# Kernel tuning notes

Hardware: AMD Instinct MI355X
Metric: run time of the kernel (lower is better)

The kernel has to match this reference:

```python
import jax, jax.numpy as jnp
import numpy as np

TEMP = 0.5
EPS = 1e-8  # torch CosineSimilarity eps


def setup_inputs() -> dict:
    key = jax.random.key(0)
    k1, k2 = jax.random.split(key)
    B, D = 4096, 256
    return {
        "features1": jax.random.normal(k1, (B, D), dtype=jnp.float32),
        "features2": jax.random.normal(k2, (B, D), dtype=jnp.float32),
    }


def reference(features1, features2):
    B = features1.shape[0]
    f = jnp.concatenate([features1, features2], axis=0)  # [2B, D]
    # cosine similarity matrix via norms + GEMM (same math as broadcasted cos)
    n = jnp.sqrt(jnp.sum(f * f, axis=-1))  # [2B]
    dots = f @ f.T  # [2B, 2B]
    logits = dots / jnp.maximum(n[:, None] * n[None, :], EPS) / TEMP
    # labels = cat([arange(B), arange(B)]) -- faithful to the source module
    labels = jnp.concatenate([jnp.arange(B), jnp.arange(B)], axis=0)  # [2B]
    lse = jax.nn.logsumexp(logits, axis=1)  # [2B]
    picked = logits[jnp.arange(2 * B), labels]  # [2B]
    return jnp.mean(lse - picked)
```

## Files before the change

### kernel.cpp

```cpp
#include <hip/hip_runtime.h>
#include <hip/hip_bf16.h>
#include <math.h>


#define B_ROWS 4096
#define D_DIM  256
#define N_ROWS 8192
#define NPANEL 64
#define NTRI   2080

typedef __attribute__((ext_vector_type(8))) short short8;
typedef __attribute__((ext_vector_type(4))) float f32x4;

__device__ __forceinline__ float bf2f(unsigned short u) {
  union { unsigned int i; float f; } p; p.i = ((unsigned int)u) << 16; return p.f;
}

__global__ __launch_bounds__(256) void nt_normalize(const float* __restrict__ f1,
                                                    const float* __restrict__ f2,
                                                    unsigned short* __restrict__ G) {
  const int row  = blockIdx.x * 4 + (threadIdx.x >> 6);
  const int lane = threadIdx.x & 63;
  const float* src = (row < B_ROWS) ? (f1 + (size_t)row * D_DIM)
                                    : (f2 + (size_t)(row - B_ROWS) * D_DIM);
  float4 v = reinterpret_cast<const float4*>(src)[lane];
  float ss = v.x * v.x + v.y * v.y + v.z * v.z + v.w * v.w;
#pragma unroll
  for (int m = 1; m < 64; m <<= 1) ss += __shfl_xor(ss, m, 64);
  float scale = 1.41421356237309515f * rsqrtf(fmaxf(ss, 1e-30f));
  union { ushort4 u; __hip_bfloat16 h[4]; } p;
  p.h[0] = __float2bfloat16(v.x * scale);
  p.h[1] = __float2bfloat16(v.y * scale);
  p.h[2] = __float2bfloat16(v.z * scale);
  p.h[3] = __float2bfloat16(v.w * scale);
  reinterpret_cast<ushort4*>(G + (size_t)row * D_DIM)[lane] = p.u;
}

__global__ __launch_bounds__(256) void nt_picked(const unsigned short* __restrict__ G,
                                                 float* __restrict__ picked) {
  const int row  = blockIdx.x * 4 + (threadIdx.x >> 6);
  const int lane = threadIdx.x & 63;
  const int lbl  = (row < B_ROWS) ? row : (row - B_ROWS);
  ushort4 a = reinterpret_cast<const ushort4*>(G + (size_t)row * D_DIM)[lane];
  ushort4 b = reinterpret_cast<const ushort4*>(G + (size_t)lbl * D_DIM)[lane];
  float s = bf2f(a.x) * bf2f(b.x) + bf2f(a.y) * bf2f(b.y) +
            bf2f(a.z) * bf2f(b.z) + bf2f(a.w) * bf2f(b.w);
#pragma unroll
  for (int m = 1; m < 64; m <<= 1) s += __shfl_xor(s, m, 64);
  if (lane == 0) picked[row] = s;
}

__device__ __forceinline__ void stage_lds(const char* gsrc_base, char* lds_base,
                                          int rounds, int tid) {
  const int lane = tid & 63, wid = tid >> 6;
  for (int r = 0; r < rounds; ++r) {
    const int o  = r * 4096 + wid * 1024 + lane * 16;
    const int so = o ^ (((o >> 9) & 7) << 4);
    __builtin_amdgcn_global_load_lds(
        (const __attribute__((address_space(1))) void*)(gsrc_base + so),
        (__attribute__((address_space(3))) void*)(lds_base + r * 4096 + wid * 1024),
        16, 0, 0);
  }
}

__global__ __launch_bounds__(256, 2) void nt_gemm_tri(
    const unsigned short* __restrict__ G,
    float* __restrict__ partial)
{
  int bid = (blockIdx.x & 7) * (NTRI / 8) + (blockIdx.x >> 3);
  int rb = (int)((sqrtf(8.f * (float)bid + 1.f) - 1.f) * 0.5f);
  while ((rb + 1) * (rb + 2) / 2 <= bid) ++rb;
  while (rb * (rb + 1) / 2 > bid) --rb;
  const int cb = bid - rb * (rb + 1) / 2;

  const int tid  = threadIdx.x;
  const int lane = tid & 63;
  const int wid  = tid >> 6;
  const int wr   = wid >> 1;
  const int wc   = wid & 1;

  __shared__ short8 lds8[4096];
  char* ldsb = reinterpret_cast<char*>(lds8);
  const char* gb = reinterpret_cast<const char*>(G);

  stage_lds(gb + (size_t)rb * 128 * 512, ldsb, 16, tid);
  __syncthreads();

  short8 afrag[4][8];
  {
    const int r0 = wr * 64;
#pragma unroll
    for (int m = 0; m < 4; ++m) {
      const int row = r0 + m * 16 + (lane & 15);
      const int sw  = (row & 7) << 4;
#pragma unroll
      for (int ks = 0; ks < 8; ++ks) {
        const int off = (row * 512 + ks * 64 + ((lane >> 4) << 4)) ^ sw;
        afrag[m][ks] = *reinterpret_cast<const short8*>(ldsb + off);
      }
    }
  }
  __syncthreads();

  stage_lds(gb + (size_t)cb * 128 * 512, ldsb, 16, tid);
  f32x4 acc[4][4] = {};
  __syncthreads();

#pragma unroll
  for (int ks = 0; ks < 8; ++ks) {
    short8 bfrag[4];
#pragma unroll
    for (int n = 0; n < 4; ++n) {
      const int brow = wc * 64 + n * 16 + (lane & 15);
      const int off  = (brow * 512 + ks * 64 + ((lane >> 4) << 4)) ^ ((brow & 7) << 4);
      bfrag[n] = *reinterpret_cast<const short8*>(ldsb + off);
    }
#pragma unroll
    for (int m = 0; m < 4; ++m)
#pragma unroll
      for (int n = 0; n < 4; ++n)
        acc[m][n] = __builtin_amdgcn_mfma_f32_16x16x32_bf16(
            afrag[m][ks], bfrag[n], acc[m][n], 0, 0, 0);
  }

  float rs[16], cs[4];
#pragma unroll
  for (int i = 0; i < 16; ++i) rs[i] = 0.f;
#pragma unroll
  for (int n = 0; n < 4; ++n) cs[n] = 0.f;
#pragma unroll
  for (int m = 0; m < 4; ++m)
#pragma unroll
    for (int n = 0; n < 4; ++n)
#pragma unroll
      for (int j = 0; j < 4; ++j) {
        const float e = __expf(acc[m][n][j]);
        rs[m * 4 + j] += e;
        cs[n] += e;
      }
#pragma unroll
  for (int i = 0; i < 16; ++i) {
    float s = rs[i];
    s += __shfl_xor(s, 1, 64);
    s += __shfl_xor(s, 2, 64);
    s += __shfl_xor(s, 4, 64);
    s += __shfl_xor(s, 8, 64);
    rs[i] = s;
  }
#pragma unroll
  for (int n = 0; n < 4; ++n) {
    float s = cs[n];
    s += __shfl_xor(s, 16, 64);
    s += __shfl_xor(s, 32, 64);
    cs[n] = s;
  }
  __syncthreads();
  float* redr = reinterpret_cast<float*>(ldsb);
  float* redc = reinterpret_cast<float*>(ldsb + 1024);
  if ((lane & 15) == 0) {
    const int g = lane >> 4;
#pragma unroll
    for (int i = 0; i < 16; ++i)
      redr[wc * 128 + wr * 64 + (i >> 2) * 16 + g * 4 + (i & 3)] = rs[i];
  }
  if ((lane >> 4) == 0) {
#pragma unroll
    for (int n = 0; n < 4; ++n)
      redc[wr * 128 + wc * 64 + n * 16 + lane] = cs[n];
  }
  __syncthreads();
  if (tid < 128) {
    const float v = redr[tid] + redr[128 + tid];
    partial[(size_t)cb * N_ROWS + (size_t)rb * 128 + tid] = v;
  } else if (rb != cb) {
    const int t = tid - 128;
    const float v = redc[t] + redc[128 + t];
    partial[(size_t)rb * N_ROWS + (size_t)cb * 128 + t] = v;
  }
}

__global__ __launch_bounds__(128) void nt_finalize1(const float* __restrict__ partial,
                                                    const float* __restrict__ picked,
                                                    float* __restrict__ loss_part) {
  const int b = blockIdx.x, tid = threadIdx.x;
  const int r = b * 128 + tid;
  float s = 0.f;
#pragma unroll
  for (int c = 0; c < NPANEL; ++c) s += partial[(size_t)c * N_ROWS + r];
  float local = __logf(s) - picked[r];
#pragma unroll
  for (int m = 1; m < 64; m <<= 1) local += __shfl_xor(local, m, 64);
  __shared__ float red[2];
  if ((tid & 63) == 0) red[tid >> 6] = local;
  __syncthreads();
  if (tid == 0) loss_part[b] = red[0] + red[1];
}

__global__ __launch_bounds__(64) void nt_finalize2(const float* __restrict__ loss_part,
                                                   float* __restrict__ out) {
  const int tid = threadIdx.x;
  float v = loss_part[tid];
#pragma unroll
  for (int m = 1; m < 64; m <<= 1) v += __shfl_xor(v, m, 64);
  if (tid == 0) out[0] = v / (float)N_ROWS;
}

extern "C" void kernel_launch(void* const* d_in, const int* in_sizes, int n_in,
                              void* d_out, int out_size, void* d_ws, size_t ws_size,
                              hipStream_t stream) {
  const float* f1 = (const float*)d_in[0];
  const float* f2 = (const float*)d_in[1];
  float* out = (float*)d_out;

  char* ws = (char*)d_ws;
  unsigned short* G = (unsigned short*)ws;
  float* partial   = (float*)(ws + (size_t)4 * 1024 * 1024);
  float* picked    = (float*)(ws + (size_t)6 * 1024 * 1024);
  float* loss_part = (float*)(ws + (size_t)6 * 1024 * 1024 + 32 * 1024);

  hipLaunchKernelGGL(nt_normalize, dim3(N_ROWS / 4), dim3(256), 0, stream, f1, f2, G);
  hipLaunchKernelGGL(nt_picked,    dim3(N_ROWS / 4), dim3(256), 0, stream, G, picked);
  hipLaunchKernelGGL(nt_gemm_tri,  dim3(NTRI),       dim3(256), 0, stream, G, partial);
  hipLaunchKernelGGL(nt_finalize1, dim3(NPANEL),     dim3(128), 0, stream, partial, picked, loss_part);
  hipLaunchKernelGGL(nt_finalize2, dim3(1),          dim3(64),  0, stream, loss_part, out);
}
```

Measured before the change: 65.90 us.

## Fuse normalize with picked logits and reuse A panel across column chunks

The normalize and picked kernels are merged into one, which computes the cross-pair dot product from fp32 values held in shared memory. The diagonal picked term for the first half becomes the constant 2. The triangular GEMM now gives each block one row panel and a chunk of up to eight column panels. The A fragments stay in registers while B sub-tiles of 64 rows are double-buffered in LDS, which cuts the repeated A staging and the number of blocks. Column sums go into a larger partial buffer that the finalize kernel reduces. The grid shrinks to 512 blocks with uneven work per block, which risks load imbalance and a lower share of active CUs.

```diff
diff --git a/kernel.cpp b/kernel.cpp
--- a/kernel.cpp
+++ b/kernel.cpp
@@ -7,47 +7,41 @@
 #define D_DIM  256
 #define N_ROWS 8192
 #define NPANEL 64
-#define NTRI   2080
 
 typedef __attribute__((ext_vector_type(8))) short short8;
 typedef __attribute__((ext_vector_type(4))) float f32x4;
 
-__device__ __forceinline__ float bf2f(unsigned short u) {
-  union { unsigned int i; float f; } p; p.i = ((unsigned int)u) << 16; return p.f;
-}
-
-__global__ __launch_bounds__(256) void nt_normalize(const float* __restrict__ f1,
-                                                    const float* __restrict__ f2,
-                                                    unsigned short* __restrict__ G) {
-  const int row  = blockIdx.x * 4 + (threadIdx.x >> 6);
-  const int lane = threadIdx.x & 63;
-  const float* src = (row < B_ROWS) ? (f1 + (size_t)row * D_DIM)
-                                    : (f2 + (size_t)(row - B_ROWS) * D_DIM);
-  float4 v = reinterpret_cast<const float4*>(src)[lane];
+__global__ __launch_bounds__(256) void nt_norm_picked(
+    const float* __restrict__ f1, const float* __restrict__ f2,
+    unsigned short* __restrict__ G, float* __restrict__ picked_cross) {
+  __shared__ float4 vbuf[2][64];
+  __shared__ float ssbuf[2];
+  const int tid = threadIdx.x, lane = tid & 63, w = tid >> 6;
+  const int pl = w >> 1, src = w & 1;
+  const int p = blockIdx.x * 2 + pl;
+  const float* rowp = (src == 0 ? f1 : f2) + (size_t)p * D_DIM;
+  float4 v = reinterpret_cast<const float4*>(rowp)[lane];
   float ss = v.x * v.x + v.y * v.y + v.z * v.z + v.w * v.w;
 #pragma unroll
   for (int m = 1; m < 64; m <<= 1) ss += __shfl_xor(ss, m, 64);
-  float scale = 1.41421356237309515f * rsqrtf(fmaxf(ss, 1e-30f));
-  union { ushort4 u; __hip_bfloat16 h[4]; } p;
-  p.h[0] = __float2bfloat16(v.x * scale);
-  p.h[1] = __float2bfloat16(v.y * scale);
-  p.h[2] = __float2bfloat16(v.z * scale);
-  p.h[3] = __float2bfloat16(v.w * scale);
-  reinterpret_cast<ushort4*>(G + (size_t)row * D_DIM)[lane] = p.u;
-}
-
-__global__ __launch_bounds__(256) void nt_picked(const unsigned short* __restrict__ G,
-                                                 float* __restrict__ picked) {
-  const int row  = blockIdx.x * 4 + (threadIdx.x >> 6);
-  const int lane = threadIdx.x & 63;
-  const int lbl  = (row < B_ROWS) ? row : (row - B_ROWS);
-  ushort4 a = reinterpret_cast<const ushort4*>(G + (size_t)row * D_DIM)[lane];
-  ushort4 b = reinterpret_cast<const ushort4*>(G + (size_t)lbl * D_DIM)[lane];
-  float s = bf2f(a.x) * bf2f(b.x) + bf2f(a.y) * bf2f(b.y) +
-            bf2f(a.z) * bf2f(b.z) + bf2f(a.w) * bf2f(b.w);
-#pragma unroll
-  for (int m = 1; m < 64; m <<= 1) s += __shfl_xor(s, m, 64);
-  if (lane == 0) picked[row] = s;
+  const float scale = 1.41421356237309515f * rsqrtf(fmaxf(ss, 1e-30f));
+  union { ushort4 u; __hip_bfloat16 h[4]; } pk;
+  pk.h[0] = __float2bfloat16(v.x * scale);
+  pk.h[1] = __float2bfloat16(v.y * scale);
+  pk.h[2] = __float2bfloat16(v.z * scale);
+  pk.h[3] = __float2bfloat16(v.w * scale);
+  const int grow = p + src * B_ROWS;
+  reinterpret_cast<ushort4*>(G + (size_t)grow * D_DIM)[lane] = pk.u;
+  if (src == 0) { vbuf[pl][lane] = v; if (lane == 0) ssbuf[pl] = ss; }
+  __syncthreads();
+  if (src == 1) {
+    float4 u = vbuf[pl][lane];
+    float d = v.x * u.x + v.y * u.y + v.z * u.z + v.w * u.w;
+#pragma unroll
+    for (int m = 1; m < 64; m <<= 1) d += __shfl_xor(d, m, 64);
+    if (lane == 0)
+      picked_cross[p] = 2.0f * d * rsqrtf(ss) * rsqrtf(ssbuf[pl]);
+  }
 }
 
 __device__ __forceinline__ void stage_lds(const char* gsrc_base, char* lds_base,
@@ -67,11 +61,12 @@
     const unsigned short* __restrict__ G,
     float* __restrict__ partial)
 {
-  int bid = (blockIdx.x & 7) * (NTRI / 8) + (blockIdx.x >> 3);
-  int rb = (int)((sqrtf(8.f * (float)bid + 1.f) - 1.f) * 0.5f);
-  while ((rb + 1) * (rb + 2) / 2 <= bid) ++rb;
-  while (rb * (rb + 1) / 2 > bid) --rb;
-  const int cb = bid - rb * (rb + 1) / 2;
+  const int bid = blockIdx.x;
+  const int rb  = 63 - (bid >> 3);
+  const int ch  = bid & 7;
+  const int cb0 = ch << 3;
+  if (cb0 > rb) return;
+  const int nsub = (rb + 1 - cb0 < 8 ? rb + 1 - cb0 : 8) << 1;
 
   const int tid  = threadIdx.x;
   const int lane = tid & 63;
@@ -83,9 +78,8 @@
   char* ldsb = reinterpret_cast<char*>(lds8);
   const char* gb = reinterpret_cast<const char*>(G);
 
-  stage_lds(gb + (size_t)rb * 128 * 512, ldsb, 16, tid);
-  __syncthreads();
-
+  stage_lds(gb + (size_t)rb * 65536, ldsb, 16, tid);
+  __syncthreads();
   short8 afrag[4][8];
   {
     const int r0 = wr * 64;
@@ -102,102 +96,107 @@
   }
   __syncthreads();
 
-  stage_lds(gb + (size_t)cb * 128 * 512, ldsb, 16, tid);
-  f32x4 acc[4][4] = {};
-  __syncthreads();
-
-#pragma unroll
-  for (int ks = 0; ks < 8; ++ks) {
-    short8 bfrag[4];
-#pragma unroll
-    for (int n = 0; n < 4; ++n) {
-      const int brow = wc * 64 + n * 16 + (lane & 15);
-      const int off  = (brow * 512 + ks * 64 + ((lane >> 4) << 4)) ^ ((brow & 7) << 4);
-      bfrag[n] = *reinterpret_cast<const short8*>(ldsb + off);
+  float rs[16];
+#pragma unroll
+  for (int i = 0; i < 16; ++i) rs[i] = 0.f;
+
+  stage_lds(gb + (size_t)cb0 * 65536, ldsb, 8, tid);
+  __syncthreads();
+
+  for (int s = 0; s < nsub; ++s) {
+    if (s + 1 < nsub)
+      stage_lds(gb + (size_t)cb0 * 65536 + (size_t)(s + 1) * 32768,
+                ldsb + ((s + 1) & 1) * 32768, 8, tid);
+
+    const char* bbuf = ldsb + (s & 1) * 32768;
+    f32x4 acc[4][2] = {};
+#pragma unroll
+    for (int ks = 0; ks < 8; ++ks) {
+      short8 bfrag[2];
+#pragma unroll
+      for (int n = 0; n < 2; ++n) {
+        const int brow = wc * 32 + n * 16 + (lane & 15);
+        const int off  = (brow * 512 + ks * 64 + ((lane >> 4) << 4)) ^ ((brow & 7) << 4);
+        bfrag[n] = *reinterpret_cast<const short8*>(bbuf + off);
+      }
+#pragma unroll
+      for (int m = 0; m < 4; ++m)
+#pragma unroll
+        for (int n = 0; n < 2; ++n)
+          acc[m][n] = __builtin_amdgcn_mfma_f32_16x16x32_bf16(
+              afrag[m][ks], bfrag[n], acc[m][n], 0, 0, 0);
     }
+    float cs0 = 0.f, cs1 = 0.f;
 #pragma unroll
     for (int m = 0; m < 4; ++m)
 #pragma unroll
-      for (int n = 0; n < 4; ++n)
-        acc[m][n] = __builtin_amdgcn_mfma_f32_16x16x32_bf16(
-            afrag[m][ks], bfrag[n], acc[m][n], 0, 0, 0);
-  }
-
-  float rs[16], cs[4];
-#pragma unroll
-  for (int i = 0; i < 16; ++i) rs[i] = 0.f;
-#pragma unroll
-  for (int n = 0; n < 4; ++n) cs[n] = 0.f;
-#pragma unroll
-  for (int m = 0; m < 4; ++m)
-#pragma unroll
-    for (int n = 0; n < 4; ++n)
-#pragma unroll
       for (int j = 0; j < 4; ++j) {
-        const float e = __expf(acc[m][n][j]);
-        rs[m * 4 + j] += e;
-        cs[n] += e;
-      }
+        const float e0 = __expf(acc[m][0][j]);
+        const float e1 = __expf(acc[m][1][j]);
+        rs[m * 4 + j] += e0 + e1;
+        cs0 += e0; cs1 += e1;
+      }
+    const int cb = cb0 + (s >> 1);
+    if (cb != rb) {
+      cs0 += __shfl_xor(cs0, 16, 64); cs0 += __shfl_xor(cs0, 32, 64);
+      cs1 += __shfl_xor(cs1, 16, 64); cs1 += __shfl_xor(cs1, 32, 64);
+      if (lane < 16) {
+        float* dst = partial + (size_t)(8 + 2 * rb + wr) * N_ROWS
+                   + cb0 * 128 + s * 64 + wc * 32 + lane;
+        dst[0]  = cs0;
+        dst[16] = cs1;
+      }
+    }
+    __syncthreads();
+  }
+
 #pragma unroll
   for (int i = 0; i < 16; ++i) {
-    float s = rs[i];
-    s += __shfl_xor(s, 1, 64);
-    s += __shfl_xor(s, 2, 64);
-    s += __shfl_xor(s, 4, 64);
-    s += __shfl_xor(s, 8, 64);
-    rs[i] = s;
-  }
-#pragma unroll
-  for (int n = 0; n < 4; ++n) {
-    float s = cs[n];
-    s += __shfl_xor(s, 16, 64);
-    s += __shfl_xor(s, 32, 64);
-    cs[n] = s;
+    float v = rs[i];
+    v += __shfl_xor(v, 1, 64);
+    v += __shfl_xor(v, 2, 64);
+    v += __shfl_xor(v, 4, 64);
+    v += __shfl_xor(v, 8, 64);
+    rs[i] = v;
   }
   __syncthreads();
   float* redr = reinterpret_cast<float*>(ldsb);
-  float* redc = reinterpret_cast<float*>(ldsb + 1024);
   if ((lane & 15) == 0) {
     const int g = lane >> 4;
 #pragma unroll
     for (int i = 0; i < 16; ++i)
       redr[wc * 128 + wr * 64 + (i >> 2) * 16 + g * 4 + (i & 3)] = rs[i];
   }
-  if ((lane >> 4) == 0) {
-#pragma unroll
-    for (int n = 0; n < 4; ++n)
-      redc[wr * 128 + wc * 64 + n * 16 + lane] = cs[n];
-  }
-  __syncthreads();
-  if (tid < 128) {
-    const float v = redr[tid] + redr[128 + tid];
-    partial[(size_t)cb * N_ROWS + (size_t)rb * 128 + tid] = v;
-  } else if (rb != cb) {
-    const int t = tid - 128;
-    const float v = redc[t] + redc[128 + t];
-    partial[(size_t)rb * N_ROWS + (size_t)cb * 128 + t] = v;
-  }
-}
-
-__global__ __launch_bounds__(128) void nt_finalize1(const float* __restrict__ partial,
-                                                    const float* __restrict__ picked,
-                                                    float* __restrict__ loss_part) {
-  const int b = blockIdx.x, tid = threadIdx.x;
-  const int r = b * 128 + tid;
+  __syncthreads();
+  if (tid < 128)
+    partial[(size_t)ch * N_ROWS + (size_t)rb * 128 + tid] =
+        redr[tid] + redr[128 + tid];
+}
+
+__global__ __launch_bounds__(128) void nt_finalize1(
+    const float* __restrict__ partial, const float* __restrict__ picked_cross,
+    float* __restrict__ loss_part) {
+  const int p = blockIdx.x, tid = threadIdx.x;
+  const int r = p * 128 + tid;
   float s = 0.f;
-#pragma unroll
-  for (int c = 0; c < NPANEL; ++c) s += partial[(size_t)c * N_ROWS + r];
-  float local = __logf(s) - picked[r];
+  const int chmax = p >> 3;
+  for (int ch = 0; ch <= chmax; ++ch) s += partial[(size_t)ch * N_ROWS + r];
+  for (int rb = p + 1; rb < NPANEL; ++rb) {
+    s += partial[(size_t)(8 + 2 * rb) * N_ROWS + r];
+    s += partial[(size_t)(9 + 2 * rb) * N_ROWS + r];
+  }
+  const float pick = (r < B_ROWS) ? 2.0f : picked_cross[r - B_ROWS];
+  float local = __logf(s) - pick;
 #pragma unroll
   for (int m = 1; m < 64; m <<= 1) local += __shfl_xor(local, m, 64);
   __shared__ float red[2];
   if ((tid & 63) == 0) red[tid >> 6] = local;
   __syncthreads();
-  if (tid == 0) loss_part[b] = red[0] + red[1];
-}
-
-__global__ __launch_bounds__(64) void nt_finalize2(const float* __restrict__ loss_part,
-                                                   float* __restrict__ out) {
+  if (tid == 0) loss_part[p] = red[0] + red[1];
+}
+
+__global__ __launch_bounds__(64) void nt_finalize2(
+    const float* __restrict__ loss_part, float* __restrict__ out) {
   const int tid = threadIdx.x;
   float v = loss_part[tid];
 #pragma unroll
@@ -213,14 +212,17 @@
   float* out = (float*)d_out;
 
   char* ws = (char*)d_ws;
-  unsigned short* G = (unsigned short*)ws;
-  float* partial   = (float*)(ws + (size_t)4 * 1024 * 1024);
-  float* picked    = (float*)(ws + (size_t)6 * 1024 * 1024);
-  float* loss_part = (float*)(ws + (size_t)6 * 1024 * 1024 + 32 * 1024);
-
-  hipLaunchKernelGGL(nt_normalize, dim3(N_ROWS / 4), dim3(256), 0, stream, f1, f2, G);
-  hipLaunchKernelGGL(nt_picked,    dim3(N_ROWS / 4), dim3(256), 0, stream, G, picked);
-  hipLaunchKernelGGL(nt_gemm_tri,  dim3(NTRI),       dim3(256), 0, stream, G, partial);
-  hipLaunchKernelGGL(nt_finalize1, dim3(NPANEL),     dim3(128), 0, stream, partial, picked, loss_part);
-  hipLaunchKernelGGL(nt_finalize2, dim3(1),          dim3(64),  0, stream, loss_part, out);
-}
+  unsigned short* G    = (unsigned short*)ws;
+  float* partial       = (float*)(ws + (size_t)4 * 1024 * 1024);
+  float* picked_cross  = (float*)(ws + (size_t)9 * 1024 * 1024);
+  float* loss_part     = (float*)(ws + (size_t)9 * 1024 * 1024 + 64 * 1024);
+
+  hipLaunchKernelGGL(nt_norm_picked, dim3(B_ROWS / 2), dim3(256), 0, stream,
+                     f1, f2, G, picked_cross);
+  hipLaunchKernelGGL(nt_gemm_tri, dim3(NPANEL * 8), dim3(256), 0, stream,
+                     G, partial);
+  hipLaunchKernelGGL(nt_finalize1, dim3(NPANEL), dim3(128), 0, stream,
+                     partial, picked_cross, loss_part);
+  hipLaunchKernelGGL(nt_finalize2, dim3(1), dim3(64), 0, stream,
+                     loss_part, out);
+}
```

Result: slower. 67.48 us (+2.4%).
